# Performance work log

Hardware: AMD Instinct MI355X
Metric: run time of the kernel (lower is better)

## Reference

```python
import jax, jax.numpy as jnp
import numpy as np

# Hyperparameters from __init__
TEMPERATURE = 0.07
HARD_POS_W = 1.5
HARD_NEG_W = 2.0
THR_POS = 0.5
THR_NEG = 0.3
NEG_LOSS_W = 0.3

B, D, N_CLASSES = 8192, 256, 1024


def setup_inputs() -> dict:
    key = jax.random.key(0)
    kf, kl = jax.random.split(key)
    features = jax.random.normal(kf, (B, D), dtype=jnp.float32)
    labels = jax.random.randint(kl, (B,), 0, N_CLASSES, dtype=jnp.int32)
    return {"features": features, "labels": labels}


def reference(features, labels):
    b = features.shape[0]
    # L2-normalize features (F.normalize(dim=1))
    anchor = features / jnp.linalg.norm(features, axis=1, keepdims=True)
    sim = anchor @ anchor.T                      # [B, B] cosine similarity
    logits = sim / TEMPERATURE
    logits = logits - jax.lax.stop_gradient(jnp.max(logits, axis=1, keepdims=True))

    mask = (labels[:, None] == labels[None, :]).astype(logits.dtype)   # same-class
    logits_mask = 1.0 - jnp.eye(b, dtype=logits.dtype)                 # exclude self

    # W2ML weights: computed from detached similarities (torch used .item())
    sim_d = jax.lax.stop_gradient(sim)
    offdiag = logits_mask > 0
    is_pos = mask > 0
    hard_pos = is_pos & (sim_d < THR_POS) & offdiag
    pos_weights = jnp.where(
        hard_pos, 1.0 + (THR_POS - sim_d) / THR_POS * (HARD_POS_W - 1.0), 1.0)
    hard_neg = (~is_pos) & (sim_d > THR_NEG) & offdiag
    neg_weights = jnp.where(
        hard_neg, 1.0 + (sim_d - THR_NEG) / (1.0 - THR_NEG) * (HARD_NEG_W - 1.0), 1.0)

    # SupCon log-prob with self excluded from the denominator
    exp_logits = jnp.exp(logits) * logits_mask
    denom = jnp.sum(exp_logits, axis=1, keepdims=True)
    log_prob = logits - jnp.log(denom)

    pos_mask = mask * logits_mask
    pos_cnt = jnp.clip(jnp.sum(pos_mask, axis=1), 1.0, None)
    positive_loss = -jnp.mean(
        jnp.sum(pos_mask * pos_weights * log_prob, axis=1) / pos_cnt)

    # Negative term: weighted mean probability mass assigned to negatives
    neg_mask = (1.0 - mask) * logits_mask
    neg_cnt = jnp.clip(jnp.sum(neg_mask, axis=1), 1.0, None)
    prob = exp_logits / denom
    negative_loss = jnp.mean(
        jnp.sum(neg_mask * neg_weights * prob, axis=1) / neg_cnt)

    return positive_loss + NEG_LOSS_W * negative_loss
```

## Files before the change

kernel.cpp:

```cpp
#include <hip/hip_runtime.h>

#define BSZ  8192
#define DDIM 256
#define BM 128
#define BN 128
#define NT   64
#define NTRI (NT * (NT + 1) / 2)

typedef float f32x4 __attribute__((ext_vector_type(4)));
typedef short bf16x8 __attribute__((ext_vector_type(8)));

__device__ __forceinline__ unsigned short f32_to_bf16(float f) {
    unsigned int u = __float_as_uint(f);
    u += 0x7fffu + ((u >> 16) & 1u);
    return (unsigned short)(u >> 16);
}

#if __has_builtin(__builtin_amdgcn_exp2f)
__device__ __forceinline__ float fast_exp2(float x) { return __builtin_amdgcn_exp2f(x); }
#else
__device__ __forceinline__ float fast_exp2(float x) {
    float r;
    asm("v_exp_f32 %0, %1" : "=v"(r) : "v"(x));
    return r;
}
#endif

#define K_E1   20.60992915555662f
#define K_E2  -20.60992915555662f
#define K_INVT 14.285714285714286f
#define K_N1   1.4285714285714286f
#define K_N2   0.5714285714285714f

__device__ __forceinline__ void decode_tile(int t, int& It, int& Jt) {
    const int off1 = 136, off2 = 392, off3 = 648, off4 = 904, off5 = 1040,
              off6 = 1296, off7 = 1552, off8 = 1688, off9 = 1944;
    int b = (t >= off1) + (t >= off2) + (t >= off3) + (t >= off4) + (t >= off5)
          + (t >= off6) + (t >= off7) + (t >= off8) + (t >= off9);
    int si, sj, r0;
    switch (b) {
        case 0: si = 0; sj = 0; r0 = 0;    break;
        case 1: si = 0; sj = 1; r0 = off1; break;
        case 2: si = 0; sj = 2; r0 = off2; break;
        case 3: si = 0; sj = 3; r0 = off3; break;
        case 4: si = 1; sj = 1; r0 = off4; break;
        case 5: si = 1; sj = 2; r0 = off5; break;
        case 6: si = 1; sj = 3; r0 = off6; break;
        case 7: si = 2; sj = 2; r0 = off7; break;
        case 8: si = 2; sj = 3; r0 = off8; break;
        default: si = 3; sj = 3; r0 = off9; break;
    }
    const int rr = t - r0;
    int il, jl;
    if (si == sj) {
        il = 0;
        #pragma unroll
        for (int q = 1; q < 16; q++) if (rr >= (16 * q - (q * (q - 1)) / 2)) il = q;
        jl = il + (rr - (16 * il - (il * (il - 1)) / 2));
    } else {
        il = rr >> 4;
        jl = rr & 15;
    }
    It = si * 16 + il;
    Jt = sj * 16 + jl;
}

__global__ __launch_bounds__(256) void norm_kernel(const float* __restrict__ feat,
                                                   unsigned short* __restrict__ anchorT,
                                                   float* __restrict__ posAcc,
                                                   unsigned int* __restrict__ counter) {
    __shared__ __align__(16) unsigned short img[8 * 512];
    const int tid  = threadIdx.x;
    const int wid  = tid >> 6;
    const int lane = tid & 63;
    const int R    = blockIdx.x;
    const int R0   = R * 16;

    if (tid < 64) posAcc[blockIdx.x * 64 + tid] = 0.0f;
    if (blockIdx.x == 0 && tid == 0) *counter = 0u;

    #pragma unroll
    for (int it = 0; it < 4; it++) {
        const int row = R0 + it * 4 + wid;
        const float4 v = ((const float4*)(feat + (size_t)row * DDIM))[lane];
        float ss = v.x * v.x + v.y * v.y + v.z * v.z + v.w * v.w;
        #pragma unroll
        for (int off = 32; off > 0; off >>= 1) ss += __shfl_xor(ss, off, 64);
        const float inv = rsqrtf(ss);
        ushort4 o;
        o.x = f32_to_bf16(v.x * inv);
        o.y = f32_to_bf16(v.y * inv);
        o.z = f32_to_bf16(v.z * inv);
        o.w = f32_to_bf16(v.w * inv);
        const int C    = lane >> 3;
        const int l16  = (row & 15) + (((lane >> 1) & 3) << 4);
        *(ushort4*)(&img[C * 512 + l16 * 8 + (lane & 1) * 4]) = o;
    }
    __syncthreads();
    #pragma unroll
    for (int p = 0; p < 2; p++) {
        const int c = p * 4 + wid;
        *(bf16x8*)(anchorT + ((size_t)(c * 512 + R)) * 512 + lane * 8) =
            *(const bf16x8*)(&img[c * 512 + lane * 8]);
    }
}

__device__ __forceinline__ void gload_lds16(const unsigned short* g, unsigned short* l) {
    __builtin_amdgcn_global_load_lds(
        (const __attribute__((address_space(1))) void*)g,
        (__attribute__((address_space(3))) void*)l, 16, 0, 0);
}

__global__ __launch_bounds__(512) void simloss_kernel(
    const unsigned short* __restrict__ anchorT,
    const int* __restrict__ labels,
    float* __restrict__ part,
    float* __restrict__ posAcc)
{
    __shared__ __align__(16) unsigned short As[8 * 512];
    __shared__ __align__(16) unsigned short As2[8 * 512];
    __shared__ __align__(16) unsigned short Bs[8 * 512];
    __shared__ __align__(16) unsigned short Bs2[8 * 512];
    __shared__ float rowDT[2][BM][2];
    __shared__ float colDT[4][BN][2];
    __shared__ int rowLab[BM];
    __shared__ int colLab[BN];

    int It, Jt;
    decode_tile(blockIdx.x, It, Jt);
    const bool diag = (It == Jt);
    const int I0 = It * BM, J0 = Jt * BN;

    const int tid  = threadIdx.x;
    const int lane = tid & 63;
    const int w    = tid >> 6;
    const int rw   = w >> 1;
    const int cw   = w & 1;
    const int cl   = lane & 15;
    const int rg   = lane >> 4;
    const int laneOff = lane * 8;

    if (tid < BM) rowLab[tid] = labels[I0 + tid];
    else if (tid < 2 * BM) colLab[tid - BM] = labels[J0 + tid - BM];

    f32x4 acc[2][4];
    #pragma unroll
    for (int f = 0; f < 2; f++)
        #pragma unroll
        for (int g = 0; g < 4; g++)
            acc[f][g] = (f32x4){0.f, 0.f, 0.f, 0.f};

    #pragma unroll
    for (int kc = 0; kc < 4; kc++) {
        {
            const int C0 = kc * 2;
            const size_t ga0 = ((size_t)C0 * 512 + It * 8) * 512;
            const size_t gb0 = ((size_t)C0 * 512 + Jt * 8) * 512;
            const size_t ga1 = ((size_t)(C0 + 1) * 512 + It * 8) * 512;
            const size_t gb1 = ((size_t)(C0 + 1) * 512 + Jt * 8) * 512;
            gload_lds16(anchorT + ga0 + tid * 8, &As[w * 512]);
            gload_lds16(anchorT + gb0 + tid * 8, &Bs[w * 512]);
            gload_lds16(anchorT + ga1 + tid * 8, &As2[w * 512]);
            gload_lds16(anchorT + gb1 + tid * 8, &Bs2[w * 512]);
        }
        __syncthreads();
        #pragma unroll
        for (int ks = 0; ks < 2; ks++) {
            const unsigned short* aB = (ks == 0 ? As : As2) + (rw * 2) * 512 + laneOff;
            const unsigned short* bB = (ks == 0 ? Bs : Bs2) + (cw * 4) * 512 + laneOff;
            const bf16x8 a0 = *(const bf16x8*)(aB);
            const bf16x8 a1 = *(const bf16x8*)(aB + 512);
            const bf16x8 b0 = *(const bf16x8*)(bB);
            const bf16x8 b1 = *(const bf16x8*)(bB + 512);
            const bf16x8 b2 = *(const bf16x8*)(bB + 1024);
            const bf16x8 b3 = *(const bf16x8*)(bB + 1536);
            acc[0][0] = __builtin_amdgcn_mfma_f32_16x16x32_bf16(a0, b0, acc[0][0], 0, 0, 0);
            acc[0][1] = __builtin_amdgcn_mfma_f32_16x16x32_bf16(a0, b1, acc[0][1], 0, 0, 0);
            acc[0][2] = __builtin_amdgcn_mfma_f32_16x16x32_bf16(a0, b2, acc[0][2], 0, 0, 0);
            acc[0][3] = __builtin_amdgcn_mfma_f32_16x16x32_bf16(a0, b3, acc[0][3], 0, 0, 0);
            acc[1][0] = __builtin_amdgcn_mfma_f32_16x16x32_bf16(a1, b0, acc[1][0], 0, 0, 0);
            acc[1][1] = __builtin_amdgcn_mfma_f32_16x16x32_bf16(a1, b1, acc[1][1], 0, 0, 0);
            acc[1][2] = __builtin_amdgcn_mfma_f32_16x16x32_bf16(a1, b2, acc[1][2], 0, 0, 0);
            acc[1][3] = __builtin_amdgcn_mfma_f32_16x16x32_bf16(a1, b3, acc[1][3], 0, 0, 0);
        }
        __syncthreads();
    }

    int ljr[4], gjr[4];
    #pragma unroll
    for (int g = 0; g < 4; g++) {
        const int cidx = cw * 64 + g * 16 + cl;
        ljr[g] = colLab[cidx];
        gjr[g] = J0 + cidx;
    }
    float cd[4] = {0.f, 0.f, 0.f, 0.f}, ct[4] = {0.f, 0.f, 0.f, 0.f};

    #pragma unroll
    for (int f = 0; f < 2; f++) {
        float rd[4] = {0.f, 0.f, 0.f, 0.f}, rt[4] = {0.f, 0.f, 0.f, 0.f};
        int li[4], gi[4];
        #pragma unroll
        for (int r = 0; r < 4; r++) {
            const int ridx = rw * 32 + f * 16 + rg * 4 + r;
            li[r] = rowLab[ridx];
            gi[r] = I0 + ridx;
        }
        #pragma unroll
        for (int g = 0; g < 4; g++) {
            const int lj = ljr[g];
            const bool granule = (rw * 2 + f) == (cw * 4 + g);
            const f32x4 c = acc[f][g];
            #pragma unroll
            for (int r = 0; r < 4; r++) {
                const float s = c[r];
                const bool self = diag && granule && ((rg * 4 + r) == cl);
                const float e  = self ? 0.f : fast_exp2(fmaf(s, K_E1, K_E2));
                const float wn = fmaxf(fmaf(s, K_N1, K_N2), 1.0f);
                const float we = wn * e;
                rd[r] += e;  rt[r] += we;
                if (!diag) { cd[g] += e; ct[g] += we; }
                if (li[r] == lj && !self) {
                    const float wp = fmaxf(1.5f - s, 1.0f);
                    const float slp = fmaf(s, K_INVT, -K_INVT) * wp;
                    float* pi = posAcc + (size_t)gi[r] * 4;
                    atomicAdd(pi + 0, slp);
                    atomicAdd(pi + 1, wp);
                    atomicAdd(pi + 2, we);
                    atomicAdd(pi + 3, 1.0f);
                    if (!diag) {
                        float* pj = posAcc + (size_t)gjr[g] * 4;
                        atomicAdd(pj + 0, slp);
                        atomicAdd(pj + 1, wp);
                        atomicAdd(pj + 2, we);
                        atomicAdd(pj + 3, 1.0f);
                    }
                }
            }
        }
        #pragma unroll
        for (int r = 0; r < 4; r++) {
            #pragma unroll
            for (int off = 1; off < 16; off <<= 1) {
                rd[r] += __shfl_xor(rd[r], off, 64);
                rt[r] += __shfl_xor(rt[r], off, 64);
            }
        }
        if (cl == 0) {
            #pragma unroll
            for (int r = 0; r < 4; r++) {
                const int row = rw * 32 + f * 16 + rg * 4 + r;
                rowDT[cw][row][0] = rd[r];
                rowDT[cw][row][1] = rt[r];
            }
        }
    }
    if (!diag) {
        #pragma unroll
        for (int g = 0; g < 4; g++) {
            cd[g] += __shfl_xor(cd[g], 16, 64);
            cd[g] += __shfl_xor(cd[g], 32, 64);
            ct[g] += __shfl_xor(ct[g], 16, 64);
            ct[g] += __shfl_xor(ct[g], 32, 64);
        }
        if (rg == 0) {
            #pragma unroll
            for (int g = 0; g < 4; g++) {
                const int col = cw * 64 + g * 16 + cl;
                colDT[rw][col][0] = cd[g];
                colDT[rw][col][1] = ct[g];
            }
        }
    }

    __syncthreads();
    if (tid < BM) {
        float2 v;
        v.x = rowDT[0][tid][0] + rowDT[1][tid][0];
        v.y = rowDT[0][tid][1] + rowDT[1][tid][1];
        ((float2*)part)[(size_t)Jt * BSZ + I0 + tid] = v;
    } else if (tid < 2 * BM && !diag) {
        const int c = tid - BM;
        float2 v;
        v.x = colDT[0][c][0] + colDT[1][c][0] + colDT[2][c][0] + colDT[3][c][0];
        v.y = colDT[0][c][1] + colDT[1][c][1] + colDT[2][c][1] + colDT[3][c][1];
        ((float2*)part)[(size_t)It * BSZ + J0 + c] = v;
    }
}

__global__ __launch_bounds__(256) void reduce_final_kernel(
    const float* __restrict__ part, const float* __restrict__ posAcc,
    double* __restrict__ partial, unsigned int* __restrict__ counter,
    float* __restrict__ out)
{
    const int t   = threadIdx.x;
    const int row = blockIdx.x * 32 + (t >> 3);
    const int sg  = t & 7;
    float dsum = 0.f, T2 = 0.f;
    const float2* p2 = (const float2*)part;
    #pragma unroll
    for (int j = 0; j < 8; j++) {
        const float2 v = p2[(size_t)(sg * 8 + j) * BSZ + row];
        dsum += v.x; T2 += v.y;
    }
    #pragma unroll
    for (int off = 1; off < 8; off <<= 1) {
        dsum += __shfl_xor(dsum, off, 64);
        T2   += __shfl_xor(T2,   off, 64);
    }
    __shared__ double sp[32], sn[32];
    if (sg == 0) {
        const float4 pa = ((const float4*)posAcc)[row];
        const float s1 = pa.x, w1 = pa.y, s2 = T2 - pa.z, cnt = pa.w;
        const float pc = fmaxf(cnt, 1.0f);
        const float nc = fmaxf(8191.0f - cnt, 1.0f);
        const float ld = logf(dsum);
        sp[t >> 3] = (double)((s1 - ld * w1) / pc);
        sn[t >> 3] = (double)((s2 / dsum) / nc);
    }
    __syncthreads();
    __shared__ bool amLast;
    if (t < 32) {
        double p = sp[t], n = sn[t];
        #pragma unroll
        for (int off = 1; off < 32; off <<= 1) {
            p += __shfl_xor(p, off, 64);
            n += __shfl_xor(n, off, 64);
        }
        if (t == 0) {
            partial[blockIdx.x * 2 + 0] = p;
            partial[blockIdx.x * 2 + 1] = n;
            __threadfence();
            amLast = (atomicAdd(counter, 1u) == 255u);
        }
    }
    __syncthreads();
    if (amLast) {
        __threadfence();
        __shared__ double fp[256], fn[256];
        volatile double* vp = (volatile double*)partial;
        fp[t] = vp[t * 2 + 0];
        fn[t] = vp[t * 2 + 1];
        __syncthreads();
        for (int s = 128; s > 0; s >>= 1) {
            if (t < s) { fp[t] += fp[t + s]; fn[t] += fn[t + s]; }
            __syncthreads();
        }
        if (t == 0) out[0] = (float)(-fp[0] / (double)BSZ + 0.3 * (fn[0] / (double)BSZ));
    }
}

extern "C" void kernel_launch(void* const* d_in, const int* in_sizes, int n_in,
                              void* d_out, int out_size, void* d_ws, size_t ws_size,
                              hipStream_t stream) {
    const float* feat = (const float*)d_in[0];
    const int* labels = (const int*)d_in[1];
    float* out = (float*)d_out;

    char* ws = (char*)d_ws;
    unsigned short* anchorT = (unsigned short*)ws;
    const size_t anchorBytes = (size_t)BSZ * DDIM * sizeof(unsigned short);
    float* part = (float*)(ws + anchorBytes);
    const size_t partBytes = (size_t)NT * BSZ * 2 * sizeof(float);
    float* posAcc = (float*)(ws + anchorBytes + partBytes);
    const size_t posBytes = (size_t)BSZ * 4 * sizeof(float);
    double* partial = (double*)(ws + anchorBytes + partBytes + posBytes);
    unsigned int* counter = (unsigned int*)(ws + anchorBytes + partBytes + posBytes + 4096);

    norm_kernel<<<BSZ / 16, 256, 0, stream>>>(feat, anchorT, posAcc, counter);
    simloss_kernel<<<NTRI, 512, 0, stream>>>(anchorT, labels, part, posAcc);
    reduce_final_kernel<<<BSZ / 32, 256, 0, stream>>>(part, posAcc, partial, counter, out);
}
```

Measured before the change: 117.1 us.

## Double-buffer K-chunk loads, DPP row reductions, swizzle norm LDS staging

The GEMM K loop now streams one 32-wide chunk at a time into ping-pong LDS buffers. The next chunk's global-to-LDS load is issued before computing on the current one, and manual vmcnt waits and barriers replace the full syncthreads pairs. The 16-lane row reductions use DPP adds instead of shuffles, and the norm kernel's LDS transpose uses an XOR swizzle to reduce bank conflicts. The handwritten waitcnt/barrier sequencing is fragile and could race if the counts are wrong.

Result: faster. 109.5 us (-6.5%).

```diff
diff --git a/kernel.cpp b/kernel.cpp
--- a/kernel.cpp
+++ b/kernel.cpp
@@ -31,6 +31,23 @@
 #define K_INVT 14.285714285714286f
 #define K_N1   1.4285714285714286f
 #define K_N2   0.5714285714285714f
+
+template<int CTRL>
+__device__ __forceinline__ float dpp_add(float v) {
+    int t = __builtin_amdgcn_update_dpp(0, __float_as_int(v), CTRL, 0xF, 0xF, true);
+    return v + __int_as_float(t);
+}
+__device__ __forceinline__ float red16(float v) {
+    v = dpp_add<0xB1>(v);
+    v = dpp_add<0x4E>(v);
+    v = dpp_add<0x141>(v);
+    v = dpp_add<0x140>(v);
+    return v;
+}
+
+__device__ __forceinline__ int swz(int b) {
+    return b ^ ((((b >> 7) ^ (b >> 10)) & 7) << 4);
+}
 
 __device__ __forceinline__ void decode_tile(int t, int& It, int& Jt) {
     const int off1 = 136, off2 = 392, off3 = 648, off4 = 904, off5 = 1040,
@@ -70,6 +87,7 @@
                                                    float* __restrict__ posAcc,
                                                    unsigned int* __restrict__ counter) {
     __shared__ __align__(16) unsigned short img[8 * 512];
+    char* const imgb = (char*)img;
     const int tid  = threadIdx.x;
     const int wid  = tid >> 6;
     const int lane = tid & 63;
@@ -94,14 +112,15 @@
         o.w = f32_to_bf16(v.w * inv);
         const int C    = lane >> 3;
         const int l16  = (row & 15) + (((lane >> 1) & 3) << 4);
-        *(ushort4*)(&img[C * 512 + l16 * 8 + (lane & 1) * 4]) = o;
+        const int wb   = (C << 10) + (l16 << 4) + ((lane & 1) << 3);
+        *(ushort4*)(imgb + swz(wb)) = o;
     }
     __syncthreads();
     #pragma unroll
     for (int p = 0; p < 2; p++) {
         const int c = p * 4 + wid;
         *(bf16x8*)(anchorT + ((size_t)(c * 512 + R)) * 512 + lane * 8) =
-            *(const bf16x8*)(&img[c * 512 + lane * 8]);
+            *(const bf16x8*)(imgb + swz((c << 10) + (lane << 4)));
     }
 }
 
@@ -150,40 +169,50 @@
         for (int g = 0; g < 4; g++)
             acc[f][g] = (f32x4){0.f, 0.f, 0.f, 0.f};
 
-    #pragma unroll
-    for (int kc = 0; kc < 4; kc++) {
-        {
-            const int C0 = kc * 2;
-            const size_t ga0 = ((size_t)C0 * 512 + It * 8) * 512;
-            const size_t gb0 = ((size_t)C0 * 512 + Jt * 8) * 512;
-            const size_t ga1 = ((size_t)(C0 + 1) * 512 + It * 8) * 512;
-            const size_t gb1 = ((size_t)(C0 + 1) * 512 + Jt * 8) * 512;
-            gload_lds16(anchorT + ga0 + tid * 8, &As[w * 512]);
-            gload_lds16(anchorT + gb0 + tid * 8, &Bs[w * 512]);
-            gload_lds16(anchorT + ga1 + tid * 8, &As2[w * 512]);
-            gload_lds16(anchorT + gb1 + tid * 8, &Bs2[w * 512]);
-        }
-        __syncthreads();
-        #pragma unroll
-        for (int ks = 0; ks < 2; ks++) {
-            const unsigned short* aB = (ks == 0 ? As : As2) + (rw * 2) * 512 + laneOff;
-            const unsigned short* bB = (ks == 0 ? Bs : Bs2) + (cw * 4) * 512 + laneOff;
-            const bf16x8 a0 = *(const bf16x8*)(aB);
-            const bf16x8 a1 = *(const bf16x8*)(aB + 512);
-            const bf16x8 b0 = *(const bf16x8*)(bB);
-            const bf16x8 b1 = *(const bf16x8*)(bB + 512);
-            const bf16x8 b2 = *(const bf16x8*)(bB + 1024);
-            const bf16x8 b3 = *(const bf16x8*)(bB + 1536);
-            acc[0][0] = __builtin_amdgcn_mfma_f32_16x16x32_bf16(a0, b0, acc[0][0], 0, 0, 0);
-            acc[0][1] = __builtin_amdgcn_mfma_f32_16x16x32_bf16(a0, b1, acc[0][1], 0, 0, 0);
-            acc[0][2] = __builtin_amdgcn_mfma_f32_16x16x32_bf16(a0, b2, acc[0][2], 0, 0, 0);
-            acc[0][3] = __builtin_amdgcn_mfma_f32_16x16x32_bf16(a0, b3, acc[0][3], 0, 0, 0);
-            acc[1][0] = __builtin_amdgcn_mfma_f32_16x16x32_bf16(a1, b0, acc[1][0], 0, 0, 0);
-            acc[1][1] = __builtin_amdgcn_mfma_f32_16x16x32_bf16(a1, b1, acc[1][1], 0, 0, 0);
-            acc[1][2] = __builtin_amdgcn_mfma_f32_16x16x32_bf16(a1, b2, acc[1][2], 0, 0, 0);
-            acc[1][3] = __builtin_amdgcn_mfma_f32_16x16x32_bf16(a1, b3, acc[1][3], 0, 0, 0);
-        }
-        __syncthreads();
+    const unsigned short* aSrc = anchorT + (size_t)It * 4096 + tid * 8;
+    const unsigned short* bSrc = anchorT + (size_t)Jt * 4096 + tid * 8;
+    unsigned short* const aD0 = &As[w * 512];
+    unsigned short* const aD1 = &As2[w * 512];
+    unsigned short* const bD0 = &Bs[w * 512];
+    unsigned short* const bD1 = &Bs2[w * 512];
+
+    gload_lds16(aSrc, aD0);
+    gload_lds16(bSrc, bD0);
+
+    #pragma unroll
+    for (int c = 0; c < 8; c++) {
+        if (c < 7) {
+            const size_t off = (size_t)(c + 1) * 262144;
+            gload_lds16(aSrc + off, ((c + 1) & 1) ? aD1 : aD0);
+            gload_lds16(bSrc + off, ((c + 1) & 1) ? bD1 : bD0);
+            asm volatile("s_waitcnt vmcnt(2)" ::: "memory");
+        } else {
+            asm volatile("s_waitcnt vmcnt(0)" ::: "memory");
+        }
+        __builtin_amdgcn_s_barrier();
+        __builtin_amdgcn_sched_barrier(0);
+
+        const unsigned short* aB = ((c & 1) ? As2 : As) + (rw * 2) * 512 + laneOff;
+        const unsigned short* bB = ((c & 1) ? Bs2 : Bs) + (cw * 4) * 512 + laneOff;
+        const bf16x8 a0 = *(const bf16x8*)(aB);
+        const bf16x8 a1 = *(const bf16x8*)(aB + 512);
+        const bf16x8 b0 = *(const bf16x8*)(bB);
+        const bf16x8 b1 = *(const bf16x8*)(bB + 512);
+        const bf16x8 b2 = *(const bf16x8*)(bB + 1024);
+        const bf16x8 b3 = *(const bf16x8*)(bB + 1536);
+        acc[0][0] = __builtin_amdgcn_mfma_f32_16x16x32_bf16(a0, b0, acc[0][0], 0, 0, 0);
+        acc[0][1] = __builtin_amdgcn_mfma_f32_16x16x32_bf16(a0, b1, acc[0][1], 0, 0, 0);
+        acc[0][2] = __builtin_amdgcn_mfma_f32_16x16x32_bf16(a0, b2, acc[0][2], 0, 0, 0);
+        acc[0][3] = __builtin_amdgcn_mfma_f32_16x16x32_bf16(a0, b3, acc[0][3], 0, 0, 0);
+        acc[1][0] = __builtin_amdgcn_mfma_f32_16x16x32_bf16(a1, b0, acc[1][0], 0, 0, 0);
+        acc[1][1] = __builtin_amdgcn_mfma_f32_16x16x32_bf16(a1, b1, acc[1][1], 0, 0, 0);
+        acc[1][2] = __builtin_amdgcn_mfma_f32_16x16x32_bf16(a1, b2, acc[1][2], 0, 0, 0);
+        acc[1][3] = __builtin_amdgcn_mfma_f32_16x16x32_bf16(a1, b3, acc[1][3], 0, 0, 0);
+
+        if (c < 7) {
+            asm volatile("s_waitcnt lgkmcnt(0)" ::: "memory");
+            __builtin_amdgcn_s_barrier();
+        }
     }
 
     int ljr[4], gjr[4];
@@ -239,11 +268,8 @@
         }
         #pragma unroll
         for (int r = 0; r < 4; r++) {
-            #pragma unroll
-            for (int off = 1; off < 16; off <<= 1) {
-                rd[r] += __shfl_xor(rd[r], off, 64);
-                rt[r] += __shfl_xor(rt[r], off, 64);
-            }
+            rd[r] = red16(rd[r]);
+            rt[r] = red16(rt[r]);
         }
         if (cl == 0) {
             #pragma unroll
```
